# Performance work log

Measured on AMD Instinct MI355X. Metric: run time of the kernel, lower is better.

The kernel has to match this reference:

```python
import jax, jax.numpy as jnp
import numpy as np

B, T, E, H = 4, 2048, 1024, 16
D = E // H  # head_dim = 64


def _rope_tables(seq_len, head_dim):
    # Matches torch: inv_freq over even indices, emb = cat(freqs, freqs)
    inv_freq = 1.0 / (10000.0 ** (np.arange(0, head_dim, 2, dtype=np.float32) / head_dim))
    t = np.arange(seq_len, dtype=np.float32)
    freqs = np.outer(t, inv_freq)            # [T, D/2]
    emb = np.concatenate([freqs, freqs], -1)  # [T, D]
    return jnp.asarray(np.cos(emb)), jnp.asarray(np.sin(emb))


def _apply_rope(x, cos, sin):
    # x: [B, H, T, D]; cos/sin: [T, D] -- replicates the pairwise view in the torch code
    d = x.shape[-1]
    xp = x.reshape(*x.shape[:-1], d // 2, 2)
    c = cos.reshape(cos.shape[0], d // 2, 2)  # broadcast over B,H
    s = sin.reshape(sin.shape[0], d // 2, 2)
    x1, x2 = xp[..., 0], xp[..., 1]
    out = jnp.stack((x1 * c[..., 0] - x2 * s[..., 0],
                     x2 * c[..., 1] + x1 * s[..., 1]), axis=-1)
    return out.reshape(x.shape)


def setup_inputs() -> dict:
    key = jax.random.key(0)
    k1, k2, k3 = jax.random.split(key, 3)
    x = jax.random.normal(k1, (B, T, E), dtype=jnp.float32)
    w_attn = jax.random.normal(k2, (3 * E, E), dtype=jnp.float32) * 0.02
    w_proj = jax.random.normal(k3, (E, E), dtype=jnp.float32) * 0.02
    return {"x": x, "w_attn": w_attn, "w_proj": w_proj}


def reference(x, w_attn, w_proj):
    b, t, e = x.shape
    qkv = x @ w_attn.T                              # [B, T, 3E] (torch Linear: x @ W^T)
    q, k, v = jnp.split(qkv, 3, axis=-1)
    q = q.reshape(b, t, H, D).transpose(0, 2, 1, 3)  # [B, H, T, D]
    k = k.reshape(b, t, H, D).transpose(0, 2, 1, 3)
    v = v.reshape(b, t, H, D).transpose(0, 2, 1, 3)
    cos, sin = _rope_tables(t, D)
    q = _apply_rope(q, cos, sin)
    k = _apply_rope(k, cos, sin)
    scale = 1.0 / jnp.sqrt(jnp.float32(D))
    scores = jnp.einsum("bhqd,bhkd->bhqk", q, k) * scale
    causal = jnp.tril(jnp.ones((t, t), dtype=bool))
    scores = jnp.where(causal, scores, jnp.finfo(scores.dtype).min)
    attn = jax.nn.softmax(scores, axis=-1)
    y = jnp.einsum("bhqk,bhkd->bhqd", attn, v)       # [B, H, T, D]
    y = y.transpose(0, 2, 1, 3).reshape(b, t, e)
    return y @ w_proj.T
```

## Files before the change

### kernel.cpp

```cpp
#include <hip/hip_runtime.h>
#include <hip/hip_bf16.h>

#define TB 2048
#define NH 16
#define HD 64
#define NE 1024
#define NB 4
#define BHD (NB * NH)
#define MTOK (NB * TB)

typedef __attribute__((ext_vector_type(8))) short short8;
typedef __attribute__((ext_vector_type(4))) float f32x4;
typedef __attribute__((ext_vector_type(16))) float f32x16;
typedef __attribute__((ext_vector_type(4))) unsigned int u32x4;

static __device__ __forceinline__ unsigned short f2bf(float f) {
  __hip_bfloat16 h = __float2bfloat16(f);
  return __builtin_bit_cast(unsigned short, h);
}

#define GLDS(g, l)                                                              \
  __builtin_amdgcn_global_load_lds((const __attribute__((address_space(1))) void*)(g), \
                                   (__attribute__((address_space(3))) void*)(l), 16, 0, 0)

__global__ __launch_bounds__(256) void cvt_kernel(const float* __restrict__ in,
                                                  unsigned short* __restrict__ out,
                                                  int n4) {
  int i = blockIdx.x * blockDim.x + threadIdx.x;
  if (i >= n4) return;
  float4 v = reinterpret_cast<const float4*>(in)[i];
  ushort4 o;
  o.x = f2bf(v.x); o.y = f2bf(v.y); o.z = f2bf(v.z); o.w = f2bf(v.w);
  reinterpret_cast<ushort4*>(out)[i] = o;
}

__global__ __launch_bounds__(256) void rope_tab_kernel(float2* __restrict__ tab) {
  int i = blockIdx.x * 256 + threadIdx.x;
  int t = i >> 5, j = i & 31;
  float ang = (float)t * __builtin_exp2f(-(float)j * 0.41524101186092029f);
  float sv, cv;
  sincosf(ang, &sv, &cv);
  tab[i] = make_float2(cv, sv);
}

template <int EPI>
__global__ __launch_bounds__(256) void gemm_bt(
    const unsigned short* __restrict__ Am, const unsigned short* __restrict__ Bm,
    float* __restrict__ Cout, unsigned short* __restrict__ Qo,
    unsigned short* __restrict__ Ko, unsigned short* __restrict__ Vt,
    const float2* __restrict__ Tab, int Mdim, int Ndim, int Kdim) {
  __shared__ unsigned short As[128 * 64];
  __shared__ unsigned short Bs[128 * 64];

  const int tid = threadIdx.x;
  const int lane = tid & 63;
  const int w = tid >> 6;
  const int wr = w >> 1;
  const int wc = w & 1;

  const int nwg = gridDim.x * gridDim.y;
  int bid = blockIdx.y * gridDim.x + blockIdx.x;
  const int cpx = nwg >> 3;
  bid = (bid & 7) * cpx + (bid >> 3);
  const int m0 = (bid / gridDim.x) * 128;
  const int n0 = (bid % gridDim.x) * 128;

  const int col16 = lane & 15;
  const int seg = lane >> 4;

  f32x4 acc[4][4];
#pragma unroll
  for (int i = 0; i < 4; ++i)
#pragma unroll
    for (int j = 0; j < 4; ++j) acc[i][j] = f32x4{0.f, 0.f, 0.f, 0.f};

  const int lrow = lane >> 3;
  const int jg = (lane & 7) ^ lrow;

  for (int kt = 0; kt < Kdim; kt += 64) {
#pragma unroll
    for (int i = 0; i < 4; ++i) {
      const int q = w * 4 + i;
      const int row = q * 8 + lrow;
      GLDS(Am + (size_t)(m0 + row) * Kdim + kt + jg * 8, As + q * 512);
      GLDS(Bm + (size_t)(n0 + row) * Kdim + kt + jg * 8, Bs + q * 512);
    }
    __syncthreads();
#pragma unroll
    for (int kk = 0; kk < 2; ++kk) {
      short8 af[4], bfr[4];
#pragma unroll
      for (int mi = 0; mi < 4; ++mi) {
        const int row = wr * 64 + mi * 16 + col16;
        const int ch = (kk * 4 + seg) ^ (row & 7);
        af[mi] = *reinterpret_cast<const short8*>(
            reinterpret_cast<const char*>(As) + row * 128 + ch * 16);
      }
#pragma unroll
      for (int ni = 0; ni < 4; ++ni) {
        const int row = wc * 64 + ni * 16 + col16;
        const int ch = (kk * 4 + seg) ^ (row & 7);
        bfr[ni] = *reinterpret_cast<const short8*>(
            reinterpret_cast<const char*>(Bs) + row * 128 + ch * 16);
      }
#pragma unroll
      for (int mi = 0; mi < 4; ++mi)
#pragma unroll
        for (int ni = 0; ni < 4; ++ni)
          acc[mi][ni] = __builtin_amdgcn_mfma_f32_16x16x32_bf16(af[mi], bfr[ni],
                                                                acc[mi][ni], 0, 0, 0);
    }
    __syncthreads();
  }

  if (EPI == 0) {
#pragma unroll
    for (int mi = 0; mi < 4; ++mi)
#pragma unroll
      for (int ni = 0; ni < 4; ++ni) {
        const int gn = n0 + wc * 64 + ni * 16 + col16;
#pragma unroll
        for (int r = 0; r < 4; ++r) {
          const int gm = m0 + wr * 64 + mi * 16 + seg * 4 + r;
          Cout[(size_t)gm * Ndim + gn] = acc[mi][ni][r];
        }
      }
  } else {
    const int sec = n0 >> 10;
    const int cbase = (n0 & 1023) + wc * 64;
    const int h = cbase >> 6;
#pragma unroll
    for (int mi = 0; mi < 4; ++mi)
#pragma unroll
      for (int ni = 0; ni < 4; ++ni) {
        const int d = ni * 16 + col16;
        if (sec == 2) {
          const int gm0 = m0 + wr * 64 + mi * 16 + seg * 4;
          const int b = gm0 >> 11;
          const int t0 = gm0 & 2047;
          ushort4 pv;
          pv.x = f2bf(acc[mi][ni][0]);
          pv.y = f2bf(acc[mi][ni][1]);
          pv.z = f2bf(acc[mi][ni][2]);
          pv.w = f2bf(acc[mi][ni][3]);
          const size_t vaddr = (size_t)(b * NH + h) * TB * HD + (size_t)(t0 >> 5) * 2048 +
                               ((d >> 5) * 2 + ((t0 & 31) >> 4)) * 512 +
                               ((t0 >> 3) & 1) * 256 + (d & 31) * 8 + (t0 & 7);
          *reinterpret_cast<ushort4*>(Vt + vaddr) = pv;
        } else {
          const float sgn = (d & 1) ? 1.f : -1.f;
          const int j = d & 31;
#pragma unroll
          for (int r = 0; r < 4; ++r) {
            const int gm = m0 + wr * 64 + mi * 16 + seg * 4 + r;
            const int b = gm >> 11;
            const int t = gm & 2047;
            const float v = acc[mi][ni][r];
            const float p = __shfl_xor(v, 1);
            const float2 csv = Tab[t * 32 + j];
            float rot = v * csv.x + sgn * p * csv.y;
            if (sec == 0) {
              rot *= 0.18033688011112042f;
              Qo[((size_t)(b * NH + h) * TB + t) * HD + d] = f2bf(rot);
            } else {
              const size_t kaddr = (size_t)(b * NH + h) * TB * HD +
                                   (size_t)(t >> 5) * 2048 + (d >> 4) * 512 +
                                   ((d >> 3) & 1) * 256 + (t & 31) * 8 + (d & 7);
              Ko[kaddr] = f2bf(rot);
            }
          }
        }
      }
  }
}

__global__ __launch_bounds__(256) void attn_kernel(
    const unsigned short* __restrict__ Q, const unsigned short* __restrict__ K2,
    const unsigned short* __restrict__ V2, unsigned short* __restrict__ Ao) {
  const int tid = threadIdx.x;
  const int lane = tid & 63;
  const int w = tid >> 6;
  const int bx = blockIdx.x;
  const int qt = 63 - (bx >> 4);
  const int bh = ((bx & 15) << 2) | w;
  const int q0 = qt << 5;
  const int l31 = lane & 31;
  const int hi = lane >> 5;
  const int qm = l31 - 4 * hi;

  const unsigned short* Qb = Q + (size_t)bh * TB * HD;
  const unsigned short* K2b = K2 + (size_t)bh * TB * HD;
  const unsigned short* V2b = V2 + (size_t)bh * TB * HD;
  const int fo = hi * 256 + l31 * 8;

  const int batch = bh >> 4;
  const int h = bh & 15;

#define MASKDIAG(st)                                                            \
  { _Pragma("unroll") for (int r = 0; r < 16; ++r) {                            \
      const int rowb = (r & 3) + 8 * (r >> 2);                                  \
      if (rowb > qm) st[r] = -1e30f; } }

#define PVTILE(st, V0, V1, V2x, V3)                                             \
  {                                                                             \
    unsigned int wd[8];                                                         \
    _Pragma("unroll") for (int i = 0; i < 8; ++i) {                             \
      unsigned int t_;                                                          \
      asm("v_cvt_pk_bf16_f32 %0, %1, %2"                                        \
          : "=v"(t_) : "v"(st[2 * i]), "v"(st[2 * i + 1]));                     \
      wd[i] = t_;                                                               \
    }                                                                           \
    asm("v_permlane32_swap_b32 %0, %1" : "+v"(wd[0]), "+v"(wd[2]));             \
    asm("v_permlane32_swap_b32 %0, %1" : "+v"(wd[1]), "+v"(wd[3]));             \
    asm("v_permlane32_swap_b32 %0, %1" : "+v"(wd[4]), "+v"(wd[6]));             \
    asm("v_permlane32_swap_b32 %0, %1" : "+v"(wd[5]), "+v"(wd[7]));             \
    u32x4 f0 = {wd[0], wd[1], wd[2], wd[3]};                                    \
    u32x4 f1 = {wd[4], wd[5], wd[6], wd[7]};                                    \
    short8 p0 = __builtin_bit_cast(short8, f0);                                 \
    short8 p1 = __builtin_bit_cast(short8, f1);                                 \
    __builtin_amdgcn_s_setprio(1);                                              \
    o0 = __builtin_amdgcn_mfma_f32_32x32x16_bf16(V0, p0, o0, 0, 0, 0);          \
    o1 = __builtin_amdgcn_mfma_f32_32x32x16_bf16(V1, p0, o1, 0, 0, 0);          \
    o0 = __builtin_amdgcn_mfma_f32_32x32x16_bf16(V2x, p1, o0, 0, 0, 0);         \
    o1 = __builtin_amdgcn_mfma_f32_32x32x16_bf16(V3, p1, o1, 0, 0, 0);          \
    __builtin_amdgcn_s_setprio(0);                                              \
  }

  short8 qf[4];
#pragma unroll
  for (int s = 0; s < 4; ++s)
    qf[s] = *reinterpret_cast<const short8*>(
        Qb + (size_t)(q0 + l31) * HD + hi * 8 + s * 16);

  f32x16 o0, o1;
#pragma unroll
  for (int r = 0; r < 16; ++r) { o0[r] = 0.f; o1[r] = 0.f; }
  float mrow = -1e30f, lsum = 0.f;

  short8 kf0[4], kf1[4];
#pragma unroll
  for (int s = 0; s < 4; ++s)
    kf0[s] = *reinterpret_cast<const short8*>(K2b + s * 512 + fo);
  if (q0 >= 32)
#pragma unroll
    for (int s = 0; s < 4; ++s)
      kf1[s] = *reinterpret_cast<const short8*>(K2b + 2048 + s * 512 + fo);

  const int LI = qt >> 1;
  for (int kt = 0; kt <= LI; ++kt) {
    const int kv0 = kt << 6;
    const bool two = (kv0 + 32 <= q0);

    f32x16 s0, s1;
#pragma unroll
    for (int r = 0; r < 16; ++r) { s0[r] = 0.f; s1[r] = 0.f; }
    __builtin_amdgcn_s_setprio(1);
#pragma unroll
    for (int s = 0; s < 4; ++s)
      s0 = __builtin_amdgcn_mfma_f32_32x32x16_bf16(kf0[s], qf[s], s0, 0, 0, 0);
    if (two)
#pragma unroll
      for (int s = 0; s < 4; ++s)
        s1 = __builtin_amdgcn_mfma_f32_32x32x16_bf16(kf1[s], qf[s], s1, 0, 0, 0);
    __builtin_amdgcn_s_setprio(0);

    const unsigned short* Va = V2b + (size_t)(2 * kt) * 2048 + fo;
    short8 va0 = *reinterpret_cast<const short8*>(Va);
    short8 va1 = *reinterpret_cast<const short8*>(Va + 1024);
    short8 va2 = *reinterpret_cast<const short8*>(Va + 512);
    short8 va3 = *reinterpret_cast<const short8*>(Va + 1536);
    short8 vb0, vb1, vb2, vb3;
    if (two) {
      const unsigned short* Vbp = Va + 2048;
      vb0 = *reinterpret_cast<const short8*>(Vbp);
      vb1 = *reinterpret_cast<const short8*>(Vbp + 1024);
      vb2 = *reinterpret_cast<const short8*>(Vbp + 512);
      vb3 = *reinterpret_cast<const short8*>(Vbp + 1536);
    }

    if (kt < LI) {
      const unsigned short* Kn = K2b + (size_t)(2 * kt + 2) * 2048;
#pragma unroll
      for (int s = 0; s < 4; ++s)
        kf0[s] = *reinterpret_cast<const short8*>(Kn + s * 512 + fo);
      if (kv0 + 96 <= q0)
#pragma unroll
        for (int s = 0; s < 4; ++s)
          kf1[s] = *reinterpret_cast<const short8*>(Kn + 2048 + s * 512 + fo);
    }

    if (kv0 == q0) MASKDIAG(s0);
    if (two && (kv0 + 32 == q0)) MASKDIAG(s1);

    float mx[8];
#pragma unroll
    for (int i = 0; i < 8; ++i) mx[i] = fmaxf(s0[2 * i], s0[2 * i + 1]);
    if (two)
#pragma unroll
      for (int i = 0; i < 8; ++i)
        mx[i] = fmaxf(mx[i], fmaxf(s1[2 * i], s1[2 * i + 1]));
#pragma unroll
    for (int i = 0; i < 4; ++i) mx[i] = fmaxf(mx[i], mx[i + 4]);
    float pm = fmaxf(fmaxf(mx[0], mx[1]), fmaxf(mx[2], mx[3]));
    pm = fmaxf(pm, __shfl_xor(pm, 32));
    if (!__all(pm - mrow <= 8.f)) {
      const float mn = fmaxf(mrow, pm);
      const float fs = __builtin_exp2f(mrow - mn);
      mrow = mn;
      lsum *= fs;
#pragma unroll
      for (int r = 0; r < 16; ++r) { o0[r] *= fs; o1[r] *= fs; }
    }
    float sm[8];
#pragma unroll
    for (int i = 0; i < 8; ++i) {
      s0[2 * i] = __builtin_exp2f(s0[2 * i] - mrow);
      s0[2 * i + 1] = __builtin_exp2f(s0[2 * i + 1] - mrow);
      sm[i] = s0[2 * i] + s0[2 * i + 1];
    }
    if (two)
#pragma unroll
      for (int i = 0; i < 8; ++i) {
        s1[2 * i] = __builtin_exp2f(s1[2 * i] - mrow);
        s1[2 * i + 1] = __builtin_exp2f(s1[2 * i + 1] - mrow);
        sm[i] += s1[2 * i] + s1[2 * i + 1];
      }
#pragma unroll
    for (int i = 0; i < 4; ++i) sm[i] += sm[i + 4];
    float rs = (sm[0] + sm[1]) + (sm[2] + sm[3]);
    rs += __shfl_xor(rs, 32);
    lsum += rs;

    PVTILE(s0, va0, va1, va2, va3);
    if (two) PVTILE(s1, vb0, vb1, vb2, vb3);
  }

  const float inv = 1.f / lsum;
  unsigned short* Aor = Ao + ((size_t)(batch * TB + q0 + l31)) * NE + (h << 6);
#pragma unroll
  for (int dt = 0; dt < 2; ++dt) {
#pragma unroll
    for (int qd = 0; qd < 4; ++qd) {
      ushort4 pk;
      pk.x = f2bf((dt ? o1[4 * qd + 0] : o0[4 * qd + 0]) * inv);
      pk.y = f2bf((dt ? o1[4 * qd + 1] : o0[4 * qd + 1]) * inv);
      pk.z = f2bf((dt ? o1[4 * qd + 2] : o0[4 * qd + 2]) * inv);
      pk.w = f2bf((dt ? o1[4 * qd + 3] : o0[4 * qd + 3]) * inv);
      *reinterpret_cast<ushort4*>(Aor + dt * 32 + 8 * qd + 4 * hi) = pk;
    }
  }
#undef MASKDIAG
#undef PVTILE
}

extern "C" void kernel_launch(void* const* d_in, const int* in_sizes, int n_in,
                              void* d_out, int out_size, void* d_ws, size_t ws_size,
                              hipStream_t stream) {
  const float* x = (const float*)d_in[0];
  const float* w_attn = (const float*)d_in[1];
  const float* w_proj = (const float*)d_in[2];
  float* out = (float*)d_out;
  char* ws = (char*)d_ws;

  const size_t SZ_XB = (size_t)MTOK * NE * 2;
  const size_t SZ_WA = (size_t)3 * NE * NE * 2;
  const size_t SZ_WP = (size_t)NE * NE * 2;
  const size_t SZ_T = (size_t)BHD * TB * HD * 2;

  unsigned short* xb = (unsigned short*)(ws);
  unsigned short* wab = (unsigned short*)(ws + SZ_XB);
  unsigned short* wpb = (unsigned short*)(ws + SZ_XB + SZ_WA);
  unsigned short* Qs = (unsigned short*)(ws + SZ_XB + SZ_WA + SZ_WP);
  unsigned short* K2 = (unsigned short*)(ws + SZ_XB + SZ_WA + SZ_WP + SZ_T);
  unsigned short* V2 = (unsigned short*)(ws + SZ_XB + SZ_WA + SZ_WP + 2 * SZ_T);
  unsigned short* Ao = (unsigned short*)(ws + SZ_XB + SZ_WA + SZ_WP + 3 * SZ_T);
  float2* tab = (float2*)Ao;

  hipLaunchKernelGGL(cvt_kernel, dim3(MTOK * NE / 4 / 256), dim3(256), 0, stream,
                     x, xb, MTOK * NE / 4);
  hipLaunchKernelGGL(cvt_kernel, dim3(3 * NE * NE / 4 / 256), dim3(256), 0, stream,
                     w_attn, wab, 3 * NE * NE / 4);
  hipLaunchKernelGGL(cvt_kernel, dim3(NE * NE / 4 / 256), dim3(256), 0, stream,
                     w_proj, wpb, NE * NE / 4);
  hipLaunchKernelGGL(rope_tab_kernel, dim3(TB * 32 / 256), dim3(256), 0, stream, tab);

  hipLaunchKernelGGL((gemm_bt<1>), dim3(3 * NE / 128, MTOK / 128), dim3(256), 0,
                     stream, xb, wab, nullptr, Qs, K2, V2, tab, MTOK, 3 * NE, NE);

  hipLaunchKernelGGL(attn_kernel, dim3(1024), dim3(256), 0, stream,
                     Qs, K2, V2, Ao);

  hipLaunchKernelGGL((gemm_bt<0>), dim3(NE / 128, MTOK / 128), dim3(256), 0,
                     stream, Ao, wpb, out, nullptr, nullptr, nullptr,
                     (const float2*)nullptr, MTOK, NE, NE);
}
```

Before: 200.9 us.

## Triple-buffer GEMM K-loop with async LDS prefetch two tiles ahead

Replaces the single-buffered 64-wide K tile loop in the projection GEMMs with a three-stage ring of 32-wide K tiles. Global-to-LDS loads are issued two iterations ahead, and partial vmcnt waits plus one barrier per iteration replace the two full syncthreads. The aim is to overlap global memory latency with MFMA work. In exchange it uses more LDS per block, which can lower occupancy, and it halves the MFMA work done between barriers.

```diff
diff --git a/kernel.cpp b/kernel.cpp
--- a/kernel.cpp
+++ b/kernel.cpp
@@ -49,8 +49,8 @@
     float* __restrict__ Cout, unsigned short* __restrict__ Qo,
     unsigned short* __restrict__ Ko, unsigned short* __restrict__ Vt,
     const float2* __restrict__ Tab, int Mdim, int Ndim, int Kdim) {
-  __shared__ unsigned short As[128 * 64];
-  __shared__ unsigned short Bs[128 * 64];
+  __shared__ unsigned short As[3][4096];
+  __shared__ unsigned short Bs[3][4096];
 
   const int tid = threadIdx.x;
   const int lane = tid & 63;
@@ -74,44 +74,69 @@
 #pragma unroll
     for (int j = 0; j < 4; ++j) acc[i][j] = f32x4{0.f, 0.f, 0.f, 0.f};
 
-  const int lrow = lane >> 3;
-  const int jg = (lane & 7) ^ lrow;
-
-  for (int kt = 0; kt < Kdim; kt += 64) {
-#pragma unroll
-    for (int i = 0; i < 4; ++i) {
-      const int q = w * 4 + i;
-      const int row = q * 8 + lrow;
-      GLDS(Am + (size_t)(m0 + row) * Kdim + kt + jg * 8, As + q * 512);
-      GLDS(Bm + (size_t)(n0 + row) * Kdim + kt + jg * 8, Bs + q * 512);
-    }
-    __syncthreads();
-#pragma unroll
-    for (int kk = 0; kk < 2; ++kk) {
-      short8 af[4], bfr[4];
-#pragma unroll
-      for (int mi = 0; mi < 4; ++mi) {
-        const int row = wr * 64 + mi * 16 + col16;
-        const int ch = (kk * 4 + seg) ^ (row & 7);
-        af[mi] = *reinterpret_cast<const short8*>(
-            reinterpret_cast<const char*>(As) + row * 128 + ch * 16);
-      }
-#pragma unroll
-      for (int ni = 0; ni < 4; ++ni) {
-        const int row = wc * 64 + ni * 16 + col16;
-        const int ch = (kk * 4 + seg) ^ (row & 7);
-        bfr[ni] = *reinterpret_cast<const short8*>(
-            reinterpret_cast<const char*>(Bs) + row * 128 + ch * 16);
-      }
-#pragma unroll
-      for (int mi = 0; mi < 4; ++mi)
-#pragma unroll
-        for (int ni = 0; ni < 4; ++ni)
-          acc[mi][ni] = __builtin_amdgcn_mfma_f32_16x16x32_bf16(af[mi], bfr[ni],
-                                                                acc[mi][ni], 0, 0, 0);
-    }
-    __syncthreads();
-  }
+  const int NKT = Kdim >> 5;
+
+#define STAGE32(bb, tt)                                                         \
+  {                                                                             \
+    _Pragma("unroll") for (int i_ = 0; i_ < 2; ++i_) {                          \
+      const int c_ = i_ * 256 + tid;                           \
+      const int p_ = c_ >> 3;                               \
+      const int j_ = (c_ & 7) ^ (p_ & 7);                                       \
+      const int row_ = p_ * 2 + (j_ & 1);                                       \
+      const int ch_ = j_ >> 1;                            \
+      GLDS(Am + (size_t)(m0 + row_) * Kdim + (tt) * 32 + ch_ * 8,               \
+           &As[bb][c_ * 8]);                                                    \
+      GLDS(Bm + (size_t)(n0 + row_) * Kdim + (tt) * 32 + ch_ * 8,               \
+           &Bs[bb][c_ * 8]);                                                    \
+    }                                                                           \
+  }
+
+#define GITER(tt, bc, bs)                                                       \
+  {                                                                             \
+    const int tp_ = ((tt) + 2 < NKT) ? (tt) + 2 : NKT - 1;                      \
+    STAGE32(bs, tp_);                                                           \
+    short8 af[4], bf2[4];                                                       \
+    _Pragma("unroll") for (int mi = 0; mi < 4; ++mi) {                          \
+      const int row = wr * 64 + mi * 16 + col16;                                \
+      af[mi] = *reinterpret_cast<const short8*>(                                \
+          reinterpret_cast<const char*>(&As[bc][0]) + (row >> 1) * 128 +        \
+          ((((seg << 1) | (row & 1)) ^ ((row >> 1) & 7)) << 4));                \
+    }                                                                           \
+    _Pragma("unroll") for (int ni = 0; ni < 4; ++ni) {                          \
+      const int row = wc * 64 + ni * 16 + col16;                                \
+      bf2[ni] = *reinterpret_cast<const short8*>(                               \
+          reinterpret_cast<const char*>(&Bs[bc][0]) + (row >> 1) * 128 +        \
+          ((((seg << 1) | (row & 1)) ^ ((row >> 1) & 7)) << 4));                \
+    }                                                                           \
+    _Pragma("unroll") for (int mi = 0; mi < 4; ++mi)                            \
+      _Pragma("unroll") for (int ni = 0; ni < 4; ++ni)                          \
+        acc[mi][ni] = __builtin_amdgcn_mfma_f32_16x16x32_bf16(                  \
+            af[mi], bf2[ni], acc[mi][ni], 0, 0, 0);                             \
+    asm volatile("s_waitcnt vmcnt(4) lgkmcnt(0)" ::: "memory");                 \
+    __builtin_amdgcn_sched_barrier(0);                                          \
+    __builtin_amdgcn_s_barrier();                                               \
+    __builtin_amdgcn_sched_barrier(0);                                          \
+  }
+
+  STAGE32(0, 0);
+  STAGE32(1, 1);
+  asm volatile("s_waitcnt vmcnt(4)" ::: "memory");
+  __builtin_amdgcn_sched_barrier(0);
+  __builtin_amdgcn_s_barrier();
+  __builtin_amdgcn_sched_barrier(0);
+
+  int t = 0;
+  for (; t + 3 <= NKT; t += 3) {
+    GITER(t, 0, 2);
+    GITER(t + 1, 1, 0);
+    GITER(t + 2, 2, 1);
+  }
+  for (; t < NKT; ++t) {
+    const int b_ = t % 3, s_ = (t + 2) % 3;
+    GITER(t, b_, s_);
+  }
+#undef STAGE32
+#undef GITER
 
   if (EPI == 0) {
 #pragma unroll
@@ -154,18 +179,18 @@
           for (int r = 0; r < 4; ++r) {
             const int gm = m0 + wr * 64 + mi * 16 + seg * 4 + r;
             const int b = gm >> 11;
-            const int t = gm & 2047;
+            const int t2 = gm & 2047;
             const float v = acc[mi][ni][r];
             const float p = __shfl_xor(v, 1);
-            const float2 csv = Tab[t * 32 + j];
+            const float2 csv = Tab[t2 * 32 + j];
             float rot = v * csv.x + sgn * p * csv.y;
             if (sec == 0) {
               rot *= 0.18033688011112042f;
-              Qo[((size_t)(b * NH + h) * TB + t) * HD + d] = f2bf(rot);
+              Qo[((size_t)(b * NH + h) * TB + t2) * HD + d] = f2bf(rot);
             } else {
               const size_t kaddr = (size_t)(b * NH + h) * TB * HD +
-                                   (size_t)(t >> 5) * 2048 + (d >> 4) * 512 +
-                                   ((d >> 3) & 1) * 256 + (t & 31) * 8 + (d & 7);
+                                   (size_t)(t2 >> 5) * 2048 + (d >> 4) * 512 +
+                                   ((d >> 3) & 1) * 256 + (t2 & 31) * 8 + (d & 7);
               Ko[kaddr] = f2bf(rot);
             }
           }
```

Result: slower. 243.0 us (+21.0%).

## Pre-swizzle GEMM operands into MFMA fragment layout and drop LDS staging

Applied to the files above, without the earlier changes.

The conversion kernels and the attention output now write bf16 operands in a fragment-major layout, so each wave can load its MFMA fragments straight from global memory with one 16-byte load per lane. The GEMM no longer stages tiles in LDS and no longer calls __syncthreads. Instead it double-buffers fragments in registers and raises wave priority around the MFMA blocks. This removes the LDS traffic and barrier cost, but gives up sharing of tiles within a block, so the A and B fragments are each read from global or L2 memory by two waves.

```diff
diff --git a/kernel.cpp b/kernel.cpp
--- a/kernel.cpp
+++ b/kernel.cpp
@@ -19,19 +19,18 @@
   return __builtin_bit_cast(unsigned short, h);
 }
 
-#define GLDS(g, l)                                                              \
-  __builtin_amdgcn_global_load_lds((const __attribute__((address_space(1))) void*)(g), \
-                                   (__attribute__((address_space(3))) void*)(l), 16, 0, 0)
-
-__global__ __launch_bounds__(256) void cvt_kernel(const float* __restrict__ in,
-                                                  unsigned short* __restrict__ out,
-                                                  int n4) {
-  int i = blockIdx.x * blockDim.x + threadIdx.x;
-  if (i >= n4) return;
-  float4 v = reinterpret_cast<const float4*>(in)[i];
+__global__ __launch_bounds__(256) void cvt_frag_kernel(const float* __restrict__ in,
+                                                       unsigned short* __restrict__ out) {
+  const int b = blockIdx.x;
+  const int t = threadIdx.x;
+  const int row = (b >> 4) * 16 + (t >> 4);
+  const int k = (b & 15) * 64 + (t & 15) * 4;
+  float4 v = *reinterpret_cast<const float4*>(in + (size_t)row * 1024 + k);
   ushort4 o;
   o.x = f2bf(v.x); o.y = f2bf(v.y); o.z = f2bf(v.z); o.w = f2bf(v.w);
-  reinterpret_cast<ushort4*>(out)[i] = o;
+  const size_t dst = ((size_t)(row >> 4) * 32 + (k >> 5)) * 512 +
+                     ((k & 31) >> 3) * 128 + (row & 15) * 8 + (k & 7);
+  *reinterpret_cast<ushort4*>(out + dst) = o;
 }
 
 __global__ __launch_bounds__(256) void rope_tab_kernel(float2* __restrict__ tab) {
@@ -44,98 +43,85 @@
 }
 
 template <int EPI>
-__global__ __launch_bounds__(256) void gemm_bt(
-    const unsigned short* __restrict__ Am, const unsigned short* __restrict__ Bm,
+__global__ __launch_bounds__(256) void gemm_frag(
+    const unsigned short* __restrict__ A2, const unsigned short* __restrict__ B2,
     float* __restrict__ Cout, unsigned short* __restrict__ Qo,
     unsigned short* __restrict__ Ko, unsigned short* __restrict__ Vt,
-    const float2* __restrict__ Tab, int Mdim, int Ndim, int Kdim) {
-  __shared__ unsigned short As[128 * 64];
-  __shared__ unsigned short Bs[128 * 64];
-
+    const float2* __restrict__ Tab, int Ndim) {
   const int tid = threadIdx.x;
   const int lane = tid & 63;
   const int w = tid >> 6;
-  const int wr = w >> 1;
-  const int wc = w & 1;
-
-  const int nwg = gridDim.x * gridDim.y;
-  int bid = blockIdx.y * gridDim.x + blockIdx.x;
-  const int cpx = nwg >> 3;
+
+  int bid = blockIdx.x;
+  const int cpx = (int)gridDim.x >> 3;
   bid = (bid & 7) * cpx + (bid >> 3);
-  const int m0 = (bid / gridDim.x) * 128;
-  const int n0 = (bid % gridDim.x) * 128;
+  const int BNB = Ndim >> 7;
+  const int mw = (bid / BNB) * 2 + (w >> 1);
+  const int nw = (bid % BNB) * 2 + (w & 1);
 
   const int col16 = lane & 15;
   const int seg = lane >> 4;
 
+  const unsigned short* Ab = A2 + (size_t)mw * 128 * 512 + lane * 8;
+  const unsigned short* Bb = B2 + (size_t)nw * 128 * 512 + lane * 8;
+
   f32x4 acc[4][4];
 #pragma unroll
   for (int i = 0; i < 4; ++i)
 #pragma unroll
     for (int j = 0; j < 4; ++j) acc[i][j] = f32x4{0.f, 0.f, 0.f, 0.f};
 
-  const int lrow = lane >> 3;
-  const int jg = (lane & 7) ^ lrow;
-
-  for (int kt = 0; kt < Kdim; kt += 64) {
-#pragma unroll
-    for (int i = 0; i < 4; ++i) {
-      const int q = w * 4 + i;
-      const int row = q * 8 + lrow;
-      GLDS(Am + (size_t)(m0 + row) * Kdim + kt + jg * 8, As + q * 512);
-      GLDS(Bm + (size_t)(n0 + row) * Kdim + kt + jg * 8, Bs + q * 512);
-    }
-    __syncthreads();
-#pragma unroll
-    for (int kk = 0; kk < 2; ++kk) {
-      short8 af[4], bfr[4];
-#pragma unroll
-      for (int mi = 0; mi < 4; ++mi) {
-        const int row = wr * 64 + mi * 16 + col16;
-        const int ch = (kk * 4 + seg) ^ (row & 7);
-        af[mi] = *reinterpret_cast<const short8*>(
-            reinterpret_cast<const char*>(As) + row * 128 + ch * 16);
-      }
+#define LDF(D, S, KB)                                                           \
+  _Pragma("unroll") for (int q_ = 0; q_ < 4; ++q_)                              \
+      D[q_] = *reinterpret_cast<const short8*>((S) + (size_t)(q_ * 32 + (KB)) * 512);
+
+#define MFMA16(AF, BF)                                                          \
+  __builtin_amdgcn_s_setprio(1);                                                \
+  _Pragma("unroll") for (int mi_ = 0; mi_ < 4; ++mi_)                           \
+      _Pragma("unroll") for (int ni_ = 0; ni_ < 4; ++ni_)                       \
+          acc[mi_][ni_] = __builtin_amdgcn_mfma_f32_16x16x32_bf16(              \
+              AF[mi_], BF[ni_], acc[mi_][ni_], 0, 0, 0);                        \
+  __builtin_amdgcn_s_setprio(0);
+
+  short8 aA[4], bA[4], aB[4], bB[4];
+  LDF(aA, Ab, 0);
+  LDF(bA, Bb, 0);
+#pragma unroll
+  for (int kb = 0; kb < 32; kb += 2) {
+    LDF(aB, Ab, kb + 1);
+    LDF(bB, Bb, kb + 1);
+    MFMA16(aA, bA);
+    if (kb + 2 < 32) {
+      LDF(aA, Ab, kb + 2);
+      LDF(bA, Bb, kb + 2);
+    }
+    MFMA16(aB, bB);
+  }
+#undef LDF
+#undef MFMA16
+
+  if (EPI == 0) {
+#pragma unroll
+    for (int mi = 0; mi < 4; ++mi)
 #pragma unroll
       for (int ni = 0; ni < 4; ++ni) {
-        const int row = wc * 64 + ni * 16 + col16;
-        const int ch = (kk * 4 + seg) ^ (row & 7);
-        bfr[ni] = *reinterpret_cast<const short8*>(
-            reinterpret_cast<const char*>(Bs) + row * 128 + ch * 16);
-      }
-#pragma unroll
-      for (int mi = 0; mi < 4; ++mi)
-#pragma unroll
-        for (int ni = 0; ni < 4; ++ni)
-          acc[mi][ni] = __builtin_amdgcn_mfma_f32_16x16x32_bf16(af[mi], bfr[ni],
-                                                                acc[mi][ni], 0, 0, 0);
-    }
-    __syncthreads();
-  }
-
-  if (EPI == 0) {
-#pragma unroll
-    for (int mi = 0; mi < 4; ++mi)
-#pragma unroll
-      for (int ni = 0; ni < 4; ++ni) {
-        const int gn = n0 + wc * 64 + ni * 16 + col16;
+        const int gn = nw * 64 + ni * 16 + col16;
 #pragma unroll
         for (int r = 0; r < 4; ++r) {
-          const int gm = m0 + wr * 64 + mi * 16 + seg * 4 + r;
+          const int gm = mw * 64 + mi * 16 + seg * 4 + r;
           Cout[(size_t)gm * Ndim + gn] = acc[mi][ni][r];
         }
       }
   } else {
-    const int sec = n0 >> 10;
-    const int cbase = (n0 & 1023) + wc * 64;
-    const int h = cbase >> 6;
+    const int sec = nw >> 4;
+    const int h = nw & 15;
 #pragma unroll
     for (int mi = 0; mi < 4; ++mi)
 #pragma unroll
       for (int ni = 0; ni < 4; ++ni) {
         const int d = ni * 16 + col16;
         if (sec == 2) {
-          const int gm0 = m0 + wr * 64 + mi * 16 + seg * 4;
+          const int gm0 = mw * 64 + mi * 16 + seg * 4;
           const int b = gm0 >> 11;
           const int t0 = gm0 & 2047;
           ushort4 pv;
@@ -152,7 +138,7 @@
           const int j = d & 31;
 #pragma unroll
           for (int r = 0; r < 4; ++r) {
-            const int gm = m0 + wr * 64 + mi * 16 + seg * 4 + r;
+            const int gm = mw * 64 + mi * 16 + seg * 4 + r;
             const int b = gm >> 11;
             const int t = gm & 2047;
             const float v = acc[mi][ni][r];
@@ -336,7 +322,7 @@
   }
 
   const float inv = 1.f / lsum;
-  unsigned short* Aor = Ao + ((size_t)(batch * TB + q0 + l31)) * NE + (h << 6);
+  const int rb16 = ((batch * TB + q0) >> 4) + (l31 >> 4);
 #pragma unroll
   for (int dt = 0; dt < 2; ++dt) {
 #pragma unroll
@@ -346,7 +332,9 @@
       pk.y = f2bf((dt ? o1[4 * qd + 1] : o0[4 * qd + 1]) * inv);
       pk.z = f2bf((dt ? o1[4 * qd + 2] : o0[4 * qd + 2]) * inv);
       pk.w = f2bf((dt ? o1[4 * qd + 3] : o0[4 * qd + 3]) * inv);
-      *reinterpret_cast<ushort4*>(Aor + dt * 32 + 8 * qd + 4 * hi) = pk;
+      const size_t off = ((size_t)rb16 * 32 + 2 * h + dt) * 512 +
+                         qd * 128 + (l31 & 15) * 8 + 4 * hi;
+      *reinterpret_cast<ushort4*>(Ao + off) = pk;
     }
   }
 #undef MASKDIAG
@@ -367,30 +355,27 @@
   const size_t SZ_WP = (size_t)NE * NE * 2;
   const size_t SZ_T = (size_t)BHD * TB * HD * 2;
 
-  unsigned short* xb = (unsigned short*)(ws);
-  unsigned short* wab = (unsigned short*)(ws + SZ_XB);
-  unsigned short* wpb = (unsigned short*)(ws + SZ_XB + SZ_WA);
+  unsigned short* A2x = (unsigned short*)(ws);
+  unsigned short* B2wa = (unsigned short*)(ws + SZ_XB);
+  unsigned short* B2wp = (unsigned short*)(ws + SZ_XB + SZ_WA);
   unsigned short* Qs = (unsigned short*)(ws + SZ_XB + SZ_WA + SZ_WP);
   unsigned short* K2 = (unsigned short*)(ws + SZ_XB + SZ_WA + SZ_WP + SZ_T);
   unsigned short* V2 = (unsigned short*)(ws + SZ_XB + SZ_WA + SZ_WP + 2 * SZ_T);
-  unsigned short* Ao = (unsigned short*)(ws + SZ_XB + SZ_WA + SZ_WP + 3 * SZ_T);
-  float2* tab = (float2*)Ao;
-
-  hipLaunchKernelGGL(cvt_kernel, dim3(MTOK * NE / 4 / 256), dim3(256), 0, stream,
-                     x, xb, MTOK * NE / 4);
-  hipLaunchKernelGGL(cvt_kernel, dim3(3 * NE * NE / 4 / 256), dim3(256), 0, stream,
-                     w_attn, wab, 3 * NE * NE / 4);
-  hipLaunchKernelGGL(cvt_kernel, dim3(NE * NE / 4 / 256), dim3(256), 0, stream,
-                     w_proj, wpb, NE * NE / 4);
+  unsigned short* Ao2 = (unsigned short*)(ws + SZ_XB + SZ_WA + SZ_WP + 3 * SZ_T);
+  float2* tab = (float2*)Ao2;
+
+  hipLaunchKernelGGL(cvt_frag_kernel, dim3(MTOK), dim3(256), 0, stream, x, A2x);
+  hipLaunchKernelGGL(cvt_frag_kernel, dim3(3 * NE), dim3(256), 0, stream, w_attn, B2wa);
+  hipLaunchKernelGGL(cvt_frag_kernel, dim3(NE), dim3(256), 0, stream, w_proj, B2wp);
   hipLaunchKernelGGL(rope_tab_kernel, dim3(TB * 32 / 256), dim3(256), 0, stream, tab);
 
-  hipLaunchKernelGGL((gemm_bt<1>), dim3(3 * NE / 128, MTOK / 128), dim3(256), 0,
-                     stream, xb, wab, nullptr, Qs, K2, V2, tab, MTOK, 3 * NE, NE);
+  hipLaunchKernelGGL((gemm_frag<1>), dim3(64 * 24), dim3(256), 0, stream,
+                     A2x, B2wa, nullptr, Qs, K2, V2, tab, 3 * NE);
 
   hipLaunchKernelGGL(attn_kernel, dim3(1024), dim3(256), 0, stream,
-                     Qs, K2, V2, Ao);
-
-  hipLaunchKernelGGL((gemm_bt<0>), dim3(NE / 128, MTOK / 128), dim3(256), 0,
-                     stream, Ao, wpb, out, nullptr, nullptr, nullptr,
-                     (const float2*)nullptr, MTOK, NE, NE);
-}
+                     Qs, K2, V2, Ao2);
+
+  hipLaunchKernelGGL((gemm_frag<0>), dim3(64 * 8), dim3(256), 0, stream,
+                     Ao2, B2wp, out, nullptr, nullptr, nullptr,
+                     (const float2*)nullptr, NE);
+}
```

Measured after the change: 212.9 us. 6.0% more time.
